# Optimization experiments

Measured on AMD Instinct MI355X. Metric: run time of the kernel, lower is better.

Reference implementation:

```python
import jax, jax.numpy as jnp
import numpy as np

NUM_TOKENS = 8192
HIDDEN = 4096
TOTAL_EXPERTS = 512
TOP_K = 12
ROUTED_SCALING_FACTOR = 2.5


def setup_inputs() -> dict:
    key = jax.random.key(0)
    k1, k2, k3 = jax.random.split(key, 3)
    hidden_states = jax.random.normal(k1, (NUM_TOKENS, HIDDEN), dtype=jnp.float32)
    # HF layout: classifier.weight is [total_experts, hidden_size]
    classifier_weight = jax.random.normal(k2, (TOTAL_EXPERTS, HIDDEN), dtype=jnp.float32) * (HIDDEN ** -0.5)
    e_score_correction_bias = jax.random.normal(k3, (TOTAL_EXPERTS,), dtype=jnp.float32) * 0.02
    return {
        "hidden_states": hidden_states,
        "classifier_weight": classifier_weight,
        "e_score_correction_bias": e_score_correction_bias,
    }


def reference(hidden_states, classifier_weight, e_score_correction_bias):
    # Linear (no bias): [T, H] @ [H, E] -> [T, E]
    router_logits = jnp.einsum("th,eh->te", hidden_states, classifier_weight)
    router_probs = jax.nn.softmax(router_logits, axis=-1)
    # Bias only affects expert SELECTION, not the routing weights.
    biased = router_probs + e_score_correction_bias  # [T, E]
    _, selected_experts = jax.lax.top_k(biased, TOP_K)  # [T, K] int32
    # Gather original (unbiased) probs at the selected experts.
    routing_weights = jnp.take_along_axis(router_probs, selected_experts, axis=-1)  # [T, K]
    routing_weights = routing_weights * jnp.float32(ROUTED_SCALING_FACTOR)
    return routing_weights, selected_experts
```

## Files before the change

kernel.cpp:

```cpp
#include <hip/hip_runtime.h>
#include <math.h>

#define T_TOKENS 8192
#define HID      4096
#define NEXP     512
#define TOPK     12
#define RSCALE   2.5f


__device__ __forceinline__ unsigned int fkey(float f) {
    unsigned int u = __float_as_uint(f);
    return (u & 0x80000000u) ? ~u : (u | 0x80000000u);
}

__device__ __forceinline__ float pick8(const float* p, int j) {
    float v = p[0];
    if (j == 1) v = p[1];
    if (j == 2) v = p[2];
    if (j == 3) v = p[3];
    if (j == 4) v = p[4];
    if (j == 5) v = p[5];
    if (j == 6) v = p[6];
    if (j == 7) v = p[7];
    return v;
}


typedef __attribute__((ext_vector_type(8))) _Float16 f16x8;
typedef __attribute__((ext_vector_type(4))) float    f32x4;

#define BM   128
#define BM2  64
#define BN   128
#define BKF  32
#define ROWB 144

__device__ __forceinline__ void cvt4(const float4 f, uint2& h, uint2& l) {
    _Float16 h0 = (_Float16)f.x, h1 = (_Float16)f.y;
    _Float16 h2 = (_Float16)f.z, h3 = (_Float16)f.w;
    float r0 = (f.x - (float)h0) * 4096.f;
    float r1 = (f.y - (float)h1) * 4096.f;
    float r2 = (f.z - (float)h2) * 4096.f;
    float r3 = (f.w - (float)h3) * 4096.f;
    _Float16 l0 = (_Float16)r0, l1 = (_Float16)r1;
    _Float16 l2 = (_Float16)r2, l3 = (_Float16)r3;
    union P { _Float16 q[2]; unsigned int u; } p;
    p.q[0] = h0; p.q[1] = h1; h.x = p.u;
    p.q[0] = h2; p.q[1] = h3; h.y = p.u;
    p.q[0] = l0; p.q[1] = l1; l.x = p.u;
    p.q[0] = l2; p.q[1] = l3; l.y = p.u;
}

__device__ __forceinline__ void load_lds16(const void* g, void* l) {
    __builtin_amdgcn_global_load_lds((const __attribute__((address_space(1))) void*)g,
                                     (__attribute__((address_space(3))) void*)l,
                                     16, 0, 0);
}


__global__ void wconv_kernel(const float* __restrict__ W, uint4* __restrict__ Wp) {
    const int gid = blockIdx.x * 256 + threadIdx.x;
    const int e  = gid >> 10;
    const int kc = (gid >> 3) & 127;
    const int p  = gid & 7;
    const int g  = p ^ (e & 7);
    const int kbase = kc * 32 + (g & 3) * 8;
    const float* src = W + (size_t)e * HID + kbase;
    const float4 f0 = *(const float4*)src;
    const float4 f1 = *(const float4*)(src + 4);
    const float v[8] = {f0.x, f0.y, f0.z, f0.w, f1.x, f1.y, f1.z, f1.w};

    union H { _Float16 f; unsigned short u; } cv;
    unsigned short h[8];
    if (g < 4) {
        #pragma unroll
        for (int j = 0; j < 8; j++) { cv.f = (_Float16)(v[j] * 64.f); h[j] = cv.u; }
    } else {
        #pragma unroll
        for (int j = 0; j < 8; j++) {
            const float w64 = v[j] * 64.f;
            const _Float16 hh = (_Float16)w64;
            cv.f = (_Float16)((w64 - (float)hh) * 4096.f);
            h[j] = cv.u;
        }
    }
    union O { unsigned short q[8]; uint4 u; } o;
    #pragma unroll
    for (int j = 0; j < 8; j++) o.q[j] = h[j];
    Wp[(size_t)(kc * 512 + e) * 8 + p] = o.u;
}


__launch_bounds__(256, 2)
__global__ void gemm2_kernel(const float* __restrict__ X,
                             const uint4* __restrict__ Wp,
                             float* __restrict__ logits)
{
    __shared__ __align__(16) unsigned char Xs[BM2 * ROWB];
    __shared__ __align__(16) unsigned char Ws[BN * 128];

    const int tid  = threadIdx.x;
    const int lane = tid & 63;
    const int wave = tid >> 6;

    const int x8    = blockIdx.x & 7;
    const int i64   = blockIdx.x >> 3;
    const int m_grp = x8 * 16 + (i64 >> 2);
    const int n_grp = i64 & 3;
    const int tok0  = m_grp * BM2;
    const int e0    = n_grp * BN;

    const int waveM = (wave >> 1) * 32;
    const int waveN = (wave & 1) * 64;
    const int m16   = lane & 15;
    const int q     = lane >> 4;

    const float* Xb = X + (size_t)tok0 * HID;

    const char* wsrc = (const char*)Wp + (size_t)(e0 + wave * 32) * 128 + lane * 16;
    unsigned char* wdst = Ws + (wave * 32) * 128;

    float4 px[2];
    #pragma unroll
    for (int s = 0; s < 2; s++) {
        const int flat = s * 256 + tid;
        const int row = flat >> 3, grp = flat & 7;
        px[s] = *(const float4*)&Xb[(size_t)row * HID + grp * 4];
    }

    f32x4 accH[2][4], accC[2][4];
    #pragma unroll
    for (int mi = 0; mi < 2; mi++)
        #pragma unroll
        for (int ni = 0; ni < 4; ni++) { accH[mi][ni] = (f32x4)0.f; accC[mi][ni] = (f32x4)0.f; }

    #pragma unroll 1
    for (int kc = 0; kc < HID / BKF; kc++) {
        __syncthreads();

        #pragma unroll
        for (int s = 0; s < 4; s++)
            load_lds16(wsrc + (size_t)kc * (512 * 128) + s * 1024, wdst + s * 1024);

        #pragma unroll
        for (int s = 0; s < 2; s++) {
            const int flat = s * 256 + tid;
            const int row = flat >> 3, grp = flat & 7;
            uint2 h, l;
            cvt4(px[s], h, l);
            *(uint2*)(Xs + row * ROWB + grp * 8)      = h;
            *(uint2*)(Xs + row * ROWB + 80 + grp * 8) = l;
        }
        __syncthreads();

        if (kc + 1 < HID / BKF) {
            #pragma unroll
            for (int s = 0; s < 2; s++) {
                const int flat = s * 256 + tid;
                const int row = flat >> 3, grp = flat & 7;
                px[s] = *(const float4*)&Xb[(size_t)row * HID + (kc + 1) * BKF + grp * 4];
            }
        }

        f16x8 Ah[2], Al[2], Bh[4], Bl[4];
        #pragma unroll
        for (int mi = 0; mi < 2; mi++) {
            const unsigned char* p = Xs + (waveM + mi * 16 + m16) * ROWB + q * 16;
            Ah[mi] = *(const f16x8*)p;
            Al[mi] = *(const f16x8*)(p + 80);
        }
        #pragma unroll
        for (int ni = 0; ni < 4; ni++) {
            const int row = waveN + ni * 16 + m16;
            const unsigned char* pr = Ws + row * 128;
            const int r7 = row & 7;
            Bh[ni] = *(const f16x8*)(pr + ((q ^ r7) * 16));
            Bl[ni] = *(const f16x8*)(pr + (((4 | q) ^ r7) * 16));
        }

        #pragma unroll
        for (int mi = 0; mi < 2; mi++)
            #pragma unroll
            for (int ni = 0; ni < 4; ni++) {
                accH[mi][ni] = __builtin_amdgcn_mfma_f32_16x16x32_f16(Ah[mi], Bh[ni], accH[mi][ni], 0, 0, 0);
                accC[mi][ni] = __builtin_amdgcn_mfma_f32_16x16x32_f16(Ah[mi], Bl[ni], accC[mi][ni], 0, 0, 0);
                accC[mi][ni] = __builtin_amdgcn_mfma_f32_16x16x32_f16(Al[mi], Bh[ni], accC[mi][ni], 0, 0, 0);
            }
    }

    #pragma unroll
    for (int mi = 0; mi < 2; mi++)
        #pragma unroll
        for (int ni = 0; ni < 4; ni++) {
            const int e = e0 + waveN + ni * 16 + m16;
            #pragma unroll
            for (int r = 0; r < 4; r++) {
                const int token = tok0 + waveM + mi * 16 + q * 4 + r;
                logits[(size_t)token * NEXP + e] =
                    (accH[mi][ni][r] + accC[mi][ni][r] * (1.f / 4096.f)) * (1.f / 64.f);
            }
        }
}


__launch_bounds__(256, 1)
__global__ void gemm_kernel(const float* __restrict__ X,
                            const float* __restrict__ W,
                            float* __restrict__ logits)
{
    __shared__ __align__(16) unsigned char Xs[BM * ROWB];
    __shared__ __align__(16) unsigned char Ws[BN * ROWB];

    const int tid  = threadIdx.x;
    const int lane = tid & 63;
    const int wave = tid >> 6;

    const int n_grp = blockIdx.x & 3;
    const int m_grp = blockIdx.x >> 2;
    const int tok0  = m_grp * BM;
    const int e0    = n_grp * BN;

    const int waveM = (wave >> 1) * 64;
    const int waveN = (wave & 1) * 64;
    const int m16   = lane & 15;
    const int q     = lane >> 4;

    const float* Xb = X + (size_t)tok0 * HID;
    const float* Wb = W + (size_t)e0 * HID;

    float4 px[4], pw[4];
    #pragma unroll
    for (int s = 0; s < 4; s++) {
        const int flat = s * 256 + tid;
        const int row = flat >> 3, grp = flat & 7;
        px[s] = *(const float4*)&Xb[(size_t)row * HID + grp * 4];
        pw[s] = *(const float4*)&Wb[(size_t)row * HID + grp * 4];
    }

    f32x4 accH[4][4], accC[4][4];
    #pragma unroll
    for (int mi = 0; mi < 4; mi++)
        #pragma unroll
        for (int ni = 0; ni < 4; ni++) { accH[mi][ni] = (f32x4)0.f; accC[mi][ni] = (f32x4)0.f; }

    #pragma unroll 1
    for (int k0 = 0; k0 < HID; k0 += BKF) {
        #pragma unroll
        for (int s = 0; s < 4; s++) {
            const int flat = s * 256 + tid;
            const int row = flat >> 3, grp = flat & 7;
            uint2 h, l;
            cvt4(px[s], h, l);
            *(uint2*)(Xs + row * ROWB + grp * 8)      = h;
            *(uint2*)(Xs + row * ROWB + 80 + grp * 8) = l;
            const float4 w64 = make_float4(pw[s].x * 64.f, pw[s].y * 64.f,
                                           pw[s].z * 64.f, pw[s].w * 64.f);
            cvt4(w64, h, l);
            *(uint2*)(Ws + row * ROWB + grp * 8)      = h;
            *(uint2*)(Ws + row * ROWB + 80 + grp * 8) = l;
        }
        __syncthreads();

        if (k0 + BKF < HID) {
            #pragma unroll
            for (int s = 0; s < 4; s++) {
                const int flat = s * 256 + tid;
                const int row = flat >> 3, grp = flat & 7;
                px[s] = *(const float4*)&Xb[(size_t)row * HID + (k0 + BKF) + grp * 4];
                pw[s] = *(const float4*)&Wb[(size_t)row * HID + (k0 + BKF) + grp * 4];
            }
        }

        f16x8 Ah[4], Al[4], Bh[4], Bl[4];
        #pragma unroll
        for (int mi = 0; mi < 4; mi++) {
            const unsigned char* p = Xs + (waveM + mi * 16 + m16) * ROWB + q * 16;
            Ah[mi] = *(const f16x8*)p;
            Al[mi] = *(const f16x8*)(p + 80);
        }
        #pragma unroll
        for (int ni = 0; ni < 4; ni++) {
            const unsigned char* p = Ws + (waveN + ni * 16 + m16) * ROWB + q * 16;
            Bh[ni] = *(const f16x8*)p;
            Bl[ni] = *(const f16x8*)(p + 80);
        }

        #pragma unroll
        for (int mi = 0; mi < 4; mi++)
            #pragma unroll
            for (int ni = 0; ni < 4; ni++) {
                accH[mi][ni] = __builtin_amdgcn_mfma_f32_16x16x32_f16(Ah[mi], Bh[ni], accH[mi][ni], 0, 0, 0);
                accC[mi][ni] = __builtin_amdgcn_mfma_f32_16x16x32_f16(Ah[mi], Bl[ni], accC[mi][ni], 0, 0, 0);
                accC[mi][ni] = __builtin_amdgcn_mfma_f32_16x16x32_f16(Al[mi], Bh[ni], accC[mi][ni], 0, 0, 0);
            }
        __syncthreads();
    }

    #pragma unroll
    for (int mi = 0; mi < 4; mi++)
        #pragma unroll
        for (int ni = 0; ni < 4; ni++) {
            const int e = e0 + waveN + ni * 16 + m16;
            #pragma unroll
            for (int r = 0; r < 4; r++) {
                const int token = tok0 + waveM + mi * 16 + q * 4 + r;
                logits[(size_t)token * NEXP + e] =
                    (accH[mi][ni][r] + accC[mi][ni][r] * (1.f / 4096.f)) * (1.f / 64.f);
            }
        }
}


__launch_bounds__(256, 1)
__global__ void topk_kernel(const float* __restrict__ logits,
                            const float* __restrict__ bias,
                            float* __restrict__ out)
{
    const int lane = threadIdx.x & 63;
    const int wave = threadIdx.x >> 6;
    const int tok  = blockIdx.x * 4 + wave;

    const float4 bs0 = *(const float4*)&bias[4 * lane];
    const float4 bs1 = *(const float4*)&bias[256 + 4 * lane];
    const float br[8] = {bs0.x, bs0.y, bs0.z, bs0.w, bs1.x, bs1.y, bs1.z, bs1.w};

    const float4 z0 = *(const float4*)&logits[(size_t)tok * NEXP + 4 * lane];
    const float4 z1 = *(const float4*)&logits[(size_t)tok * NEXP + 256 + 4 * lane];
    float z[8] = {z0.x, z0.y, z0.z, z0.w, z1.x, z1.y, z1.z, z1.w};

    float m = z[0];
    #pragma unroll
    for (int j = 1; j < 8; j++) m = fmaxf(m, z[j]);
    #pragma unroll
    for (int off = 32; off >= 1; off >>= 1) m = fmaxf(m, __shfl_xor(m, off));

    float p[8];
    float s = 0.f;
    #pragma unroll
    for (int j = 0; j < 8; j++) { p[j] = expf(z[j] - m); s += p[j]; }
    #pragma unroll
    for (int off = 32; off >= 1; off >>= 1) s += __shfl_xor(s, off);
    const float inv = 1.f / s;

    float pb[8], bb[8];
    #pragma unroll
    for (int j = 0; j < 8; j++) {
        pb[j] = p[j] * inv;
        bb[j] = pb[j] + br[j];
    }

    for (int kk = 0; kk < TOPK; kk++) {
        unsigned long long key = 0ull;
        #pragma unroll
        for (int j = 0; j < 8; j++) {
            int e = (j < 4) ? (4 * lane + j) : (256 + 4 * lane + (j - 4));
            unsigned long long k64 =
                ((unsigned long long)fkey(bb[j]) << 32) |
                (unsigned long long)(unsigned int)(1023 - e);
            key = (k64 > key) ? k64 : key;
        }
        #pragma unroll
        for (int off = 32; off >= 1; off >>= 1) {
            unsigned long long o = __shfl_xor(key, off);
            key = (o > key) ? o : key;
        }
        const int estar = 1023 - (int)(unsigned int)(key & 0xffffffffull);

        int lstar, jstar;
        if (estar < 256) { lstar = estar >> 2;         jstar = estar & 3; }
        else             { lstar = (estar - 256) >> 2; jstar = 4 + ((estar - 256) & 3); }

        const float pj   = pick8(pb, jstar);
        const float psel = __shfl(pj, lstar);

        if (lane == lstar) {
            if (jstar == 0) bb[0] = -INFINITY;
            if (jstar == 1) bb[1] = -INFINITY;
            if (jstar == 2) bb[2] = -INFINITY;
            if (jstar == 3) bb[3] = -INFINITY;
            if (jstar == 4) bb[4] = -INFINITY;
            if (jstar == 5) bb[5] = -INFINITY;
            if (jstar == 6) bb[6] = -INFINITY;
            if (jstar == 7) bb[7] = -INFINITY;
        }

        if (lane == 0) {
            out[(size_t)tok * TOPK + kk] = psel * RSCALE;
            out[(size_t)T_TOKENS * TOPK + (size_t)tok * TOPK + kk] = (float)estar;
        }
    }
}


#define TM   32
#define BK   16
#define EPAD (NEXP + 4)
#define XPAD 36

__launch_bounds__(256, 1)
__global__ void router_kernel(const float* __restrict__ X,
                              const float* __restrict__ W,
                              const float* __restrict__ bias,
                              float* __restrict__ out)
{
    __shared__ float Wsh[BK][EPAD];
    __shared__ float Xsh[BK][XPAD];

    const int tid  = threadIdx.x;
    const int lane = tid & 63;
    const int wave = tid >> 6;
    const int tok0 = blockIdx.x * TM;

    float acc[8][8];
    #pragma unroll
    for (int i = 0; i < 8; i++)
        #pragma unroll
        for (int j = 0; j < 8; j++) acc[i][j] = 0.f;

    const int xt = tid >> 4;
    const int xk = tid & 15;

    for (int k0 = 0; k0 < HID; k0 += BK) {
        #pragma unroll
        for (int r = 0; r < 2; r++) {
            int t = r * 16 + xt;
            Xsh[xk][t] = X[(size_t)(tok0 + t) * HID + k0 + xk];
        }
        #pragma unroll
        for (int r = 0; r < 8; r++) {
            int flat4 = r * 256 + tid;
            int e  = flat4 >> 2;
            int kq = (flat4 & 3) * 4;
            const float4 wv = *(const float4*)&W[(size_t)e * HID + k0 + kq];
            Wsh[kq + 0][e] = wv.x;
            Wsh[kq + 1][e] = wv.y;
            Wsh[kq + 2][e] = wv.z;
            Wsh[kq + 3][e] = wv.w;
        }
        __syncthreads();

        #pragma unroll
        for (int k = 0; k < BK; k++) {
            float4 b0 = *(const float4*)&Wsh[k][4 * lane];
            float4 b1 = *(const float4*)&Wsh[k][256 + 4 * lane];
            float4 a0 = *(const float4*)&Xsh[k][wave * 8];
            float4 a1 = *(const float4*)&Xsh[k][wave * 8 + 4];
            float a[8] = {a0.x, a0.y, a0.z, a0.w, a1.x, a1.y, a1.z, a1.w};
            float b[8] = {b0.x, b0.y, b0.z, b0.w, b1.x, b1.y, b1.z, b1.w};
            #pragma unroll
            for (int i = 0; i < 8; i++)
                #pragma unroll
                for (int j = 0; j < 8; j++)
                    acc[i][j] = fmaf(a[i], b[j], acc[i][j]);
        }
        __syncthreads();
    }

    const float4 bs0 = *(const float4*)&bias[4 * lane];
    const float4 bs1 = *(const float4*)&bias[256 + 4 * lane];
    const float br[8] = {bs0.x, bs0.y, bs0.z, bs0.w, bs1.x, bs1.y, bs1.z, bs1.w};

    for (int i = 0; i < 8; i++) {
        const int tok = tok0 + wave * 8 + i;

        float m = acc[i][0];
        #pragma unroll
        for (int j = 1; j < 8; j++) m = fmaxf(m, acc[i][j]);
        #pragma unroll
        for (int off = 32; off >= 1; off >>= 1) m = fmaxf(m, __shfl_xor(m, off));

        float p[8];
        float s = 0.f;
        #pragma unroll
        for (int j = 0; j < 8; j++) { p[j] = expf(acc[i][j] - m); s += p[j]; }
        #pragma unroll
        for (int off = 32; off >= 1; off >>= 1) s += __shfl_xor(s, off);
        const float inv = 1.f / s;

        float pb[8], bb[8];
        #pragma unroll
        for (int j = 0; j < 8; j++) {
            pb[j] = p[j] * inv;
            bb[j] = pb[j] + br[j];
        }

        for (int kk = 0; kk < TOPK; kk++) {
            unsigned long long key = 0ull;
            #pragma unroll
            for (int j = 0; j < 8; j++) {
                int e = (j < 4) ? (4 * lane + j) : (256 + 4 * lane + (j - 4));
                unsigned long long k64 =
                    ((unsigned long long)fkey(bb[j]) << 32) |
                    (unsigned long long)(unsigned int)(1023 - e);
                key = (k64 > key) ? k64 : key;
            }
            #pragma unroll
            for (int off = 32; off >= 1; off >>= 1) {
                unsigned long long o = __shfl_xor(key, off);
                key = (o > key) ? o : key;
            }
            const int estar = 1023 - (int)(unsigned int)(key & 0xffffffffull);

            int lstar, jstar;
            if (estar < 256) { lstar = estar >> 2;         jstar = estar & 3; }
            else             { lstar = (estar - 256) >> 2; jstar = 4 + ((estar - 256) & 3); }

            const float pj   = pick8(pb, jstar);
            const float psel = __shfl(pj, lstar);

            if (lane == lstar) {
                if (jstar == 0) bb[0] = -INFINITY;
                if (jstar == 1) bb[1] = -INFINITY;
                if (jstar == 2) bb[2] = -INFINITY;
                if (jstar == 3) bb[3] = -INFINITY;
                if (jstar == 4) bb[4] = -INFINITY;
                if (jstar == 5) bb[5] = -INFINITY;
                if (jstar == 6) bb[6] = -INFINITY;
                if (jstar == 7) bb[7] = -INFINITY;
            }

            if (lane == 0) {
                out[(size_t)tok * TOPK + kk] = psel * RSCALE;
                out[(size_t)T_TOKENS * TOPK + (size_t)tok * TOPK + kk] = (float)estar;
            }
        }
    }
}


extern "C" void kernel_launch(void* const* d_in, const int* in_sizes, int n_in,
                              void* d_out, int out_size, void* d_ws, size_t ws_size,
                              hipStream_t stream)
{
    const float* X    = (const float*)d_in[0];
    const float* W    = (const float*)d_in[1];
    const float* bias = (const float*)d_in[2];
    float* out = (float*)d_out;

    const size_t logits_bytes = (size_t)T_TOKENS * NEXP * sizeof(float);
    const size_t wp_bytes     = (size_t)NEXP * HID * 4;

    if (ws_size >= logits_bytes + wp_bytes) {
        float* logits = (float*)d_ws;
        uint4* Wp     = (uint4*)((char*)d_ws + logits_bytes);
        wconv_kernel<<<dim3(2048), dim3(256), 0, stream>>>(W, Wp);
        gemm2_kernel<<<dim3(512), dim3(256), 0, stream>>>(X, Wp, logits);
        topk_kernel<<<dim3(T_TOKENS / 4), dim3(256), 0, stream>>>(logits, bias, out);
    } else if (ws_size >= logits_bytes) {
        float* logits = (float*)d_ws;
        gemm_kernel<<<dim3(256), dim3(256), 0, stream>>>(X, W, logits);
        topk_kernel<<<dim3(T_TOKENS / 4), dim3(256), 0, stream>>>(logits, bias, out);
    } else {
        router_kernel<<<dim3(T_TOKENS / TM), dim3(256), 0, stream>>>(X, W, bias, out);
    }
}
```

Baseline: 342.7 us.

## Pipeline GEMM main loop with triple-buffered W and double-buffered X in LDS

Restructures the router GEMM main loop into a software pipeline. Weight tiles are prefetched two stages ahead into three LDS buffers through direct global-to-LDS loads, and the X tile is double-buffered. The two __syncthreads per iteration become one barrier guarded by explicit vmcnt/lgkmcnt waits, and the MFMA block runs at raised wave priority. The aim is to hide global load latency behind matrix math, at the cost of more LDS per block (which may lower occupancy) and fragile hand-tuned wait counts.

```diff
diff --git a/kernel.cpp b/kernel.cpp
--- a/kernel.cpp
+++ b/kernel.cpp
@@ -34,6 +34,7 @@
 #define BN   128
 #define BKF  32
 #define ROWB 144
+#define WBUF 16384
 
 __device__ __forceinline__ void cvt4(const float4 f, uint2& h, uint2& l) {
     _Float16 h0 = (_Float16)f.x, h1 = (_Float16)f.y;
@@ -57,6 +58,8 @@
                                      16, 0, 0);
 }
 
+#define MEMFENCE asm volatile("" ::: "memory")
+
 
 __global__ void wconv_kernel(const float* __restrict__ W, uint4* __restrict__ Wp) {
     const int gid = blockIdx.x * 256 + threadIdx.x;
@@ -96,8 +99,8 @@
                              const uint4* __restrict__ Wp,
                              float* __restrict__ logits)
 {
-    __shared__ __align__(16) unsigned char Xs[BM2 * ROWB];
-    __shared__ __align__(16) unsigned char Ws[BN * 128];
+    __shared__ __align__(16) unsigned char Xs[2][BM2 * ROWB];
+    __shared__ __align__(16) unsigned char Ws[3][WBUF];
 
     const int tid  = threadIdx.x;
     const int lane = tid & 63;
@@ -118,15 +121,38 @@
     const float* Xb = X + (size_t)tok0 * HID;
 
     const char* wsrc = (const char*)Wp + (size_t)(e0 + wave * 32) * 128 + lane * 16;
-    unsigned char* wdst = Ws + (wave * 32) * 128;
+    const int   wofs = wave * 32 * 128;
+
+    const int xrow = tid >> 3;
+    const int xgrp = tid & 7;
 
     float4 px[2];
     #pragma unroll
+    for (int s = 0; s < 2; s++)
+        px[s] = *(const float4*)&Xb[(size_t)(xrow + s * 32) * HID + xgrp * 4];
+    MEMFENCE;
+    #pragma unroll
+    for (int s = 0; s < 4; s++)
+        load_lds16(wsrc + s * 1024, &Ws[0][wofs + s * 1024]);
+    MEMFENCE;
+    #pragma unroll
     for (int s = 0; s < 2; s++) {
-        const int flat = s * 256 + tid;
-        const int row = flat >> 3, grp = flat & 7;
-        px[s] = *(const float4*)&Xb[(size_t)row * HID + grp * 4];
-    }
+        uint2 h, l;
+        cvt4(px[s], h, l);
+        *(uint2*)(&Xs[0][(xrow + s * 32) * ROWB + xgrp * 8])      = h;
+        *(uint2*)(&Xs[0][(xrow + s * 32) * ROWB + 80 + xgrp * 8]) = l;
+    }
+    MEMFENCE;
+    #pragma unroll
+    for (int s = 0; s < 2; s++)
+        px[s] = *(const float4*)&Xb[(size_t)(xrow + s * 32) * HID + BKF + xgrp * 4];
+    MEMFENCE;
+    #pragma unroll
+    for (int s = 0; s < 4; s++)
+        load_lds16(wsrc + 65536 + s * 1024, &Ws[1][wofs + s * 1024]);
+    asm volatile("s_waitcnt vmcnt(6)" ::: "memory");
+    asm volatile("s_waitcnt lgkmcnt(0)" ::: "memory");
+    __builtin_amdgcn_s_barrier();
 
     f32x4 accH[2][4], accC[2][4];
     #pragma unroll
@@ -134,50 +160,87 @@
         #pragma unroll
         for (int ni = 0; ni < 4; ni++) { accH[mi][ni] = (f32x4)0.f; accC[mi][ni] = (f32x4)0.f; }
 
+    int wr = 0;
+    int ww = 2;
+
     #pragma unroll 1
-    for (int kc = 0; kc < HID / BKF; kc++) {
-        __syncthreads();
-
-        #pragma unroll
-        for (int s = 0; s < 4; s++)
-            load_lds16(wsrc + (size_t)kc * (512 * 128) + s * 1024, wdst + s * 1024);
+    for (int kc = 0; kc < 127; kc++) {
+        const int kn = (kc + 2 < 127) ? (kc + 2) : 127;
+        const int xw = (kc + 1) & 1;
+        const int xr = kc & 1;
 
         #pragma unroll
         for (int s = 0; s < 2; s++) {
-            const int flat = s * 256 + tid;
-            const int row = flat >> 3, grp = flat & 7;
             uint2 h, l;
             cvt4(px[s], h, l);
-            *(uint2*)(Xs + row * ROWB + grp * 8)      = h;
-            *(uint2*)(Xs + row * ROWB + 80 + grp * 8) = l;
-        }
-        __syncthreads();
-
-        if (kc + 1 < HID / BKF) {
-            #pragma unroll
-            for (int s = 0; s < 2; s++) {
-                const int flat = s * 256 + tid;
-                const int row = flat >> 3, grp = flat & 7;
-                px[s] = *(const float4*)&Xb[(size_t)row * HID + (kc + 1) * BKF + grp * 4];
-            }
-        }
-
+            *(uint2*)(&Xs[xw][(xrow + s * 32) * ROWB + xgrp * 8])      = h;
+            *(uint2*)(&Xs[xw][(xrow + s * 32) * ROWB + 80 + xgrp * 8]) = l;
+        }
+        MEMFENCE;
+        #pragma unroll
+        for (int s = 0; s < 2; s++)
+            px[s] = *(const float4*)&Xb[(size_t)(xrow + s * 32) * HID + kn * BKF + xgrp * 4];
+        MEMFENCE;
+        #pragma unroll
+        for (int s = 0; s < 4; s++)
+            load_lds16(wsrc + (size_t)kn * 65536 + s * 1024, &Ws[ww][wofs + s * 1024]);
+        MEMFENCE;
+
+        const unsigned char* xbase = &Xs[xr][0];
+        const unsigned char* wbase = &Ws[wr][0];
         f16x8 Ah[2], Al[2], Bh[4], Bl[4];
         #pragma unroll
         for (int mi = 0; mi < 2; mi++) {
-            const unsigned char* p = Xs + (waveM + mi * 16 + m16) * ROWB + q * 16;
+            const unsigned char* p = xbase + (waveM + mi * 16 + m16) * ROWB + q * 16;
             Ah[mi] = *(const f16x8*)p;
             Al[mi] = *(const f16x8*)(p + 80);
         }
         #pragma unroll
         for (int ni = 0; ni < 4; ni++) {
             const int row = waveN + ni * 16 + m16;
-            const unsigned char* pr = Ws + row * 128;
+            const unsigned char* pr = wbase + row * 128;
             const int r7 = row & 7;
             Bh[ni] = *(const f16x8*)(pr + ((q ^ r7) * 16));
             Bl[ni] = *(const f16x8*)(pr + (((4 | q) ^ r7) * 16));
         }
 
+        __builtin_amdgcn_s_setprio(1);
+        #pragma unroll
+        for (int mi = 0; mi < 2; mi++)
+            #pragma unroll
+            for (int ni = 0; ni < 4; ni++) {
+                accH[mi][ni] = __builtin_amdgcn_mfma_f32_16x16x32_f16(Ah[mi], Bh[ni], accH[mi][ni], 0, 0, 0);
+                accC[mi][ni] = __builtin_amdgcn_mfma_f32_16x16x32_f16(Ah[mi], Bl[ni], accC[mi][ni], 0, 0, 0);
+                accC[mi][ni] = __builtin_amdgcn_mfma_f32_16x16x32_f16(Al[mi], Bh[ni], accC[mi][ni], 0, 0, 0);
+            }
+        __builtin_amdgcn_s_setprio(0);
+
+        asm volatile("s_waitcnt vmcnt(6)" ::: "memory");
+        asm volatile("s_waitcnt lgkmcnt(0)" ::: "memory");
+        __builtin_amdgcn_s_barrier();
+
+        wr = (wr == 2) ? 0 : wr + 1;
+        ww = (ww == 2) ? 0 : ww + 1;
+    }
+
+    {
+        const unsigned char* xbase = &Xs[1][0];
+        const unsigned char* wbase = &Ws[1][0];
+        f16x8 Ah[2], Al[2], Bh[4], Bl[4];
+        #pragma unroll
+        for (int mi = 0; mi < 2; mi++) {
+            const unsigned char* p = xbase + (waveM + mi * 16 + m16) * ROWB + q * 16;
+            Ah[mi] = *(const f16x8*)p;
+            Al[mi] = *(const f16x8*)(p + 80);
+        }
+        #pragma unroll
+        for (int ni = 0; ni < 4; ni++) {
+            const int row = waveN + ni * 16 + m16;
+            const unsigned char* pr = wbase + row * 128;
+            const int r7 = row & 7;
+            Bh[ni] = *(const f16x8*)(pr + ((q ^ r7) * 16));
+            Bl[ni] = *(const f16x8*)(pr + (((4 | q) ^ r7) * 16));
+        }
         #pragma unroll
         for (int mi = 0; mi < 2; mi++)
             #pragma unroll
```

Result: slower. 357.7 us (+4.4%).

## Double-buffer LDS in gemm2 and cache per-lane top-k keys

Applied to the files above, without the earlier changes.

The gemm2 kernel now keeps two LDS buffers for the X and W tiles. The loop is unrolled by two so the weight DMA and X conversion for the next K chunk run while the current chunk is computed, which cuts one barrier per iteration. The top-k kernel precomputes 64-bit keys once and keeps a per-lane running max, so only the lane that owned the winner rescans its eight keys. The extra LDS may lower gemm2 occupancy, and topk launch bounds are raised to allow four blocks per CU.

```diff
diff --git a/kernel.cpp b/kernel.cpp
--- a/kernel.cpp
+++ b/kernel.cpp
@@ -34,6 +34,7 @@
 #define BN   128
 #define BKF  32
 #define ROWB 144
+#define WBUF 16384
 
 __device__ __forceinline__ void cvt4(const float4 f, uint2& h, uint2& l) {
     _Float16 h0 = (_Float16)f.x, h1 = (_Float16)f.y;
@@ -91,13 +92,52 @@
 }
 
 
+#define G2_XLOAD(kcl)                                                              \
+    for (int s = 0; s < 2; s++)                                                    \
+        px[s] = *(const float4*)&Xb[(size_t)(xrow + s * 32) * HID + (kcl) * BKF + xgrp * 4];
+
+#define G2_WDMA(RB, kcl)                                                           \
+    for (int s = 0; s < 4; s++)                                                    \
+        load_lds16(wsrc + (size_t)(kcl) * 65536 + s * 1024, &Ws[RB][wofs + s * 1024]);
+
+#define G2_XCVT(RB)                                                                \
+    for (int s = 0; s < 2; s++) {                                                  \
+        uint2 h, l;                                                                \
+        cvt4(px[s], h, l);                                                         \
+        *(uint2*)(&Xs[RB][(xrow + s * 32) * ROWB + xgrp * 8])      = h;            \
+        *(uint2*)(&Xs[RB][(xrow + s * 32) * ROWB + 80 + xgrp * 8]) = l;            \
+    }
+
+#define G2_COMPUTE(RB)                                                             \
+    {                                                                              \
+        f16x8 Ah[2], Al[2], Bh[4], Bl[4];                                          \
+        for (int mi = 0; mi < 2; mi++) {                                           \
+            const unsigned char* p = &Xs[RB][(waveM + mi * 16 + m16) * ROWB + q * 16]; \
+            Ah[mi] = *(const f16x8*)p;                                             \
+            Al[mi] = *(const f16x8*)(p + 80);                                      \
+        }                                                                          \
+        for (int ni = 0; ni < 4; ni++) {                                           \
+            const int row = waveN + ni * 16 + m16;                                 \
+            const unsigned char* pr = &Ws[RB][row * 128];                          \
+            const int r7 = row & 7;                                                \
+            Bh[ni] = *(const f16x8*)(pr + ((q ^ r7) * 16));                        \
+            Bl[ni] = *(const f16x8*)(pr + (((4 | q) ^ r7) * 16));                  \
+        }                                                                          \
+        for (int mi = 0; mi < 2; mi++)                                             \
+            for (int ni = 0; ni < 4; ni++) {                                       \
+                accH[mi][ni] = __builtin_amdgcn_mfma_f32_16x16x32_f16(Ah[mi], Bh[ni], accH[mi][ni], 0, 0, 0); \
+                accC[mi][ni] = __builtin_amdgcn_mfma_f32_16x16x32_f16(Ah[mi], Bl[ni], accC[mi][ni], 0, 0, 0); \
+                accC[mi][ni] = __builtin_amdgcn_mfma_f32_16x16x32_f16(Al[mi], Bh[ni], accC[mi][ni], 0, 0, 0); \
+            }                                                                      \
+    }
+
 __launch_bounds__(256, 2)
 __global__ void gemm2_kernel(const float* __restrict__ X,
                              const uint4* __restrict__ Wp,
                              float* __restrict__ logits)
 {
-    __shared__ __align__(16) unsigned char Xs[BM2 * ROWB];
-    __shared__ __align__(16) unsigned char Ws[BN * 128];
+    __shared__ __align__(16) unsigned char Xs[2][BM2 * ROWB];
+    __shared__ __align__(16) unsigned char Ws[2][WBUF];
 
     const int tid  = threadIdx.x;
     const int lane = tid & 63;
@@ -118,74 +158,39 @@
     const float* Xb = X + (size_t)tok0 * HID;
 
     const char* wsrc = (const char*)Wp + (size_t)(e0 + wave * 32) * 128 + lane * 16;
-    unsigned char* wdst = Ws + (wave * 32) * 128;
+    const int   wofs = wave * 32 * 128;
+
+    const int xrow = tid >> 3;
+    const int xgrp = tid & 7;
+
+    f32x4 accH[2][4], accC[2][4];
+    #pragma unroll
+    for (int mi = 0; mi < 2; mi++)
+        #pragma unroll
+        for (int ni = 0; ni < 4; ni++) { accH[mi][ni] = (f32x4)0.f; accC[mi][ni] = (f32x4)0.f; }
 
     float4 px[2];
-    #pragma unroll
-    for (int s = 0; s < 2; s++) {
-        const int flat = s * 256 + tid;
-        const int row = flat >> 3, grp = flat & 7;
-        px[s] = *(const float4*)&Xb[(size_t)row * HID + grp * 4];
-    }
-
-    f32x4 accH[2][4], accC[2][4];
-    #pragma unroll
-    for (int mi = 0; mi < 2; mi++)
-        #pragma unroll
-        for (int ni = 0; ni < 4; ni++) { accH[mi][ni] = (f32x4)0.f; accC[mi][ni] = (f32x4)0.f; }
+    G2_XLOAD(0);
+    G2_WDMA(0, 0);
+    G2_XCVT(0);
+    G2_XLOAD(1);
+    __syncthreads();
 
     #pragma unroll 1
-    for (int kc = 0; kc < HID / BKF; kc++) {
+    for (int kc2 = 0; kc2 < 64; kc2++) {
+        const int kc = kc2 * 2;
+
+        G2_WDMA(1, kc + 1);
+        G2_XCVT(1);
+        { const int kn = (kc + 2 < 128) ? kc + 2 : 127; G2_XLOAD(kn); }
+        G2_COMPUTE(0);
         __syncthreads();
 
-        #pragma unroll
-        for (int s = 0; s < 4; s++)
-            load_lds16(wsrc + (size_t)kc * (512 * 128) + s * 1024, wdst + s * 1024);
-
-        #pragma unroll
-        for (int s = 0; s < 2; s++) {
-            const int flat = s * 256 + tid;
-            const int row = flat >> 3, grp = flat & 7;
-            uint2 h, l;
-            cvt4(px[s], h, l);
-            *(uint2*)(Xs + row * ROWB + grp * 8)      = h;
-            *(uint2*)(Xs + row * ROWB + 80 + grp * 8) = l;
-        }
+        { const int kw = (kc + 2 < 128) ? kc + 2 : 127; G2_WDMA(0, kw); }
+        G2_XCVT(0);
+        { const int kn = (kc + 3 < 128) ? kc + 3 : 127; G2_XLOAD(kn); }
+        G2_COMPUTE(1);
         __syncthreads();
-
-        if (kc + 1 < HID / BKF) {
-            #pragma unroll
-            for (int s = 0; s < 2; s++) {
-                const int flat = s * 256 + tid;
-                const int row = flat >> 3, grp = flat & 7;
-                px[s] = *(const float4*)&Xb[(size_t)row * HID + (kc + 1) * BKF + grp * 4];
-            }
-        }
-
-        f16x8 Ah[2], Al[2], Bh[4], Bl[4];
-        #pragma unroll
-        for (int mi = 0; mi < 2; mi++) {
-            const unsigned char* p = Xs + (waveM + mi * 16 + m16) * ROWB + q * 16;
-            Ah[mi] = *(const f16x8*)p;
-            Al[mi] = *(const f16x8*)(p + 80);
-        }
-        #pragma unroll
-        for (int ni = 0; ni < 4; ni++) {
-            const int row = waveN + ni * 16 + m16;
-            const unsigned char* pr = Ws + row * 128;
-            const int r7 = row & 7;
-            Bh[ni] = *(const f16x8*)(pr + ((q ^ r7) * 16));
-            Bl[ni] = *(const f16x8*)(pr + (((4 | q) ^ r7) * 16));
-        }
-
-        #pragma unroll
-        for (int mi = 0; mi < 2; mi++)
-            #pragma unroll
-            for (int ni = 0; ni < 4; ni++) {
-                accH[mi][ni] = __builtin_amdgcn_mfma_f32_16x16x32_f16(Ah[mi], Bh[ni], accH[mi][ni], 0, 0, 0);
-                accC[mi][ni] = __builtin_amdgcn_mfma_f32_16x16x32_f16(Ah[mi], Bl[ni], accC[mi][ni], 0, 0, 0);
-                accC[mi][ni] = __builtin_amdgcn_mfma_f32_16x16x32_f16(Al[mi], Bh[ni], accC[mi][ni], 0, 0, 0);
-            }
     }
 
     #pragma unroll
@@ -311,7 +316,7 @@
 }
 
 
-__launch_bounds__(256, 1)
+__launch_bounds__(256, 4)
 __global__ void topk_kernel(const float* __restrict__ logits,
                             const float* __restrict__ bias,
                             float* __restrict__ out)
@@ -342,23 +347,21 @@
     for (int off = 32; off >= 1; off >>= 1) s += __shfl_xor(s, off);
     const float inv = 1.f / s;
 
-    float pb[8], bb[8];
+    float pb[8];
+    unsigned long long kj[8];
     #pragma unroll
     for (int j = 0; j < 8; j++) {
         pb[j] = p[j] * inv;
-        bb[j] = pb[j] + br[j];
-    }
+        const int e = (j < 4) ? (4 * lane + j) : (256 + 4 * lane + (j - 4));
+        kj[j] = ((unsigned long long)fkey(pb[j] + br[j]) << 32) |
+                (unsigned long long)(unsigned int)(1023 - e);
+    }
+    unsigned long long lk = kj[0];
+    #pragma unroll
+    for (int j = 1; j < 8; j++) lk = (kj[j] > lk) ? kj[j] : lk;
 
     for (int kk = 0; kk < TOPK; kk++) {
-        unsigned long long key = 0ull;
-        #pragma unroll
-        for (int j = 0; j < 8; j++) {
-            int e = (j < 4) ? (4 * lane + j) : (256 + 4 * lane + (j - 4));
-            unsigned long long k64 =
-                ((unsigned long long)fkey(bb[j]) << 32) |
-                (unsigned long long)(unsigned int)(1023 - e);
-            key = (k64 > key) ? k64 : key;
-        }
+        unsigned long long key = lk;
         #pragma unroll
         for (int off = 32; off >= 1; off >>= 1) {
             unsigned long long o = __shfl_xor(key, off);
@@ -374,14 +377,18 @@
         const float psel = __shfl(pj, lstar);
 
         if (lane == lstar) {
-            if (jstar == 0) bb[0] = -INFINITY;
-            if (jstar == 1) bb[1] = -INFINITY;
-            if (jstar == 2) bb[2] = -INFINITY;
-            if (jstar == 3) bb[3] = -INFINITY;
-            if (jstar == 4) bb[4] = -INFINITY;
-            if (jstar == 5) bb[5] = -INFINITY;
-            if (jstar == 6) bb[6] = -INFINITY;
-            if (jstar == 7) bb[7] = -INFINITY;
+            if (jstar == 0) kj[0] = 0ull;
+            if (jstar == 1) kj[1] = 0ull;
+            if (jstar == 2) kj[2] = 0ull;
+            if (jstar == 3) kj[3] = 0ull;
+            if (jstar == 4) kj[4] = 0ull;
+            if (jstar == 5) kj[5] = 0ull;
+            if (jstar == 6) kj[6] = 0ull;
+            if (jstar == 7) kj[7] = 0ull;
+            unsigned long long nl = kj[0];
+            #pragma unroll
+            for (int j = 1; j < 8; j++) nl = (kj[j] > nl) ? kj[j] : nl;
+            lk = nl;
         }
 
         if (lane == 0) {
```

Measured after the change: 390.4 us. 1.14x slower.
